# Kernel optimization log

Hardware: AMD Instinct MI355X
Metric: run time of the kernel (lower is better)

## Reference

```python
import jax, jax.numpy as jnp
import numpy as np

B, N, D = 4, 4096, 256
EPS = 1e-5


def setup_inputs() -> dict:
    key = jax.random.key(0)
    ks = jax.random.split(key, 6)
    x = jax.random.normal(ks[0], (B, N, D), dtype=jnp.float32)
    coord = jax.random.normal(ks[1], (B, N, D), dtype=jnp.float32)
    ln_g = jnp.ones((D,), dtype=jnp.float32)
    ln_b = jnp.zeros((D,), dtype=jnp.float32)
    s = 1.0 / np.sqrt(D)
    w_qkv = jax.random.normal(ks[2], (D, 3 * D), dtype=jnp.float32) * s
    w_out = jax.random.normal(ks[3], (D, D), dtype=jnp.float32) * s
    b_out = jnp.zeros((D,), dtype=jnp.float32)
    return {"x": x, "coord": coord, "ln_g": ln_g, "ln_b": ln_b,
            "w_qkv": w_qkv, "w_out": w_out, "b_out": b_out}


def reference(x, coord, ln_g, ln_b, w_qkv, w_out, b_out):
    d = x.shape[-1]
    scale = d ** (-0.5)
    # LayerNorm over last dim
    mu = jnp.mean(x, axis=-1, keepdims=True)
    var = jnp.var(x, axis=-1, keepdims=True)
    nx = (x - mu) * jax.lax.rsqrt(var + EPS) * ln_g + ln_b
    # QKV projection (no bias), chunk into q,k,v
    qkv = jnp.einsum('bnd,de->bne', nx, w_qkv)
    q, k, v = jnp.split(qkv, 3, axis=-1)
    # coord bias on q and k (module does NOT split into heads)
    q = q + coord
    k = k + coord
    dots = jnp.einsum('bnd,bmd->bnm', q, k) * scale
    attn = jax.nn.softmax(dots, axis=-1)
    out = jnp.einsum('bnm,bmd->bnd', attn, v)
    return jnp.einsum('bnd,de->bne', out, w_out) + b_out
```

## Files before the change

### kernel.cpp

```cpp
#include <hip/hip_runtime.h>
#include <hip/hip_fp16.h>
#include <math.h>

constexpr int B = 4, N = 4096, D = 256;
constexpr int BN = B * N;
constexpr float EPS = 1e-5f;
constexpr float QSC2 = 0.0625f * 1.44269504088896340736f;

constexpr int SPLIT = 4;
constexpr int KVB = 32;
constexpr int NTK = (N / SPLIT) / KVB;
constexpr float THR = 8.0f;

typedef __attribute__((ext_vector_type(8))) _Float16 f16x8;
typedef __attribute__((ext_vector_type(2))) __fp16 fp16x2;
typedef __attribute__((ext_vector_type(4))) float f32x4;
typedef __attribute__((ext_vector_type(16))) float f32x16;

__device__ inline f32x4 mfma_f16(f16x8 a, f16x8 b, f32x4 c) {
  return __builtin_amdgcn_mfma_f32_16x16x32_f16(a, b, c, 0, 0, 0);
}
__device__ inline f32x16 mfma32(f16x8 a, f16x8 b, f32x16 c) {
  return __builtin_amdgcn_mfma_f32_32x32x16_f16(a, b, c, 0, 0, 0);
}
__device__ inline ushort f2h(float x) {
  __half h = __float2half(x);
  return *(ushort*)&h;
}
__device__ inline float h2f(ushort u) {
  __half h;
  *(ushort*)&h = u;
  return __half2float(h);
}
__device__ inline unsigned pkh(float a, float b) {
  fp16x2 r = __builtin_amdgcn_cvt_pkrtz(a, b);
  return *(unsigned*)&r;
}
__device__ inline void gload16(const ushort* g, ushort* l) {
  __builtin_amdgcn_global_load_lds(
      (const __attribute__((address_space(1))) void*)g,
      (__attribute__((address_space(3))) void*)l, 16, 0, 0);
}

__global__ __launch_bounds__(256) void ln_kernel(
    const float* __restrict__ x, const float* __restrict__ g,
    const float* __restrict__ bta, ushort* __restrict__ nxh,
    ushort* __restrict__ nxl) {
  const int row = blockIdx.x;
  const int t = threadIdx.x;
  const float v = x[(size_t)row * D + t];
  float s = v, ss = v * v;
#pragma unroll
  for (int o = 32; o > 0; o >>= 1) {
    s += __shfl_down(s, o);
    ss += __shfl_down(ss, o);
  }
  __shared__ float red[8];
  if ((t & 63) == 0) {
    red[t >> 6] = s;
    red[(t >> 6) + 4] = ss;
  }
  __syncthreads();
  s = red[0] + red[1] + red[2] + red[3];
  ss = red[4] + red[5] + red[6] + red[7];
  const float mu = s * (1.0f / D);
  const float var = ss * (1.0f / D) - mu * mu;
  const float rsig = rsqrtf(var + EPS);
  const float nx = (v - mu) * rsig * g[t] + bta[t];
  const ushort h = f2h(nx);
  nxh[(size_t)row * D + t] = h;
  nxl[(size_t)row * D + t] = f2h(nx - h2f(h));
}

__global__ __launch_bounds__(256) void castw_kernel(
    const float* __restrict__ w_qkv, const float* __restrict__ w_out,
    ushort* __restrict__ wt, ushort* __restrict__ wot) {
  const int id = blockIdx.x * 256 + threadIdx.x;
  if (id < 768 * 256) {
    const int n = id >> 8, k = id & 255;
    wt[id] = f2h(w_qkv[(size_t)k * 768 + n]);
  } else {
    const int j = id - 768 * 256;
    const int n = j >> 8, k = j & 255;
    wot[j] = f2h(w_out[(size_t)k * 256 + n]);
  }
}

__global__ __launch_bounds__(256, 4) void qkv_kernel(
    const ushort* __restrict__ nxh, const ushort* __restrict__ nxl,
    const ushort* __restrict__ wt, const float* __restrict__ coord,
    ushort* __restrict__ qfp, ushort* __restrict__ kfp,
    ushort* __restrict__ vtp) {
  const int t = threadIdx.x;
  const int w = t >> 6, lane = t & 63;
  const int lrow = lane & 15, lhi = lane >> 4;
  const int m0 = blockIdx.x * 128 + w * 32;
  const int c0 = blockIdx.y * 64;
  f32x4 acc[2][4];
#pragma unroll
  for (int qs = 0; qs < 2; ++qs)
#pragma unroll
    for (int nt = 0; nt < 4; ++nt) acc[qs][nt] = f32x4{0.f, 0.f, 0.f, 0.f};

#pragma unroll
  for (int kc = 0; kc < D; kc += 32) {
    f16x8 ah[2], al[2], bw[4];
#pragma unroll
    for (int qs = 0; qs < 2; ++qs) {
      const size_t ao = (size_t)(m0 + qs * 16 + lrow) * D + kc + lhi * 8;
      ah[qs] = *(const f16x8*)(nxh + ao);
      al[qs] = *(const f16x8*)(nxl + ao);
    }
#pragma unroll
    for (int nt = 0; nt < 4; ++nt)
      bw[nt] = *(const f16x8*)(wt + (size_t)(c0 + nt * 16 + lrow) * D + kc +
                               lhi * 8);
#pragma unroll
    for (int qs = 0; qs < 2; ++qs)
#pragma unroll
      for (int nt = 0; nt < 4; ++nt) {
        acc[qs][nt] = mfma_f16(ah[qs], bw[nt], acc[qs][nt]);
        acc[qs][nt] = mfma_f16(al[qs], bw[nt], acc[qs][nt]);
      }
  }

  const int region = blockIdx.y >> 2;
  const int cbase = c0 & 255;
  if (region < 2) {
    const float sc = (region == 0) ? QSC2 : 1.0f;
    ushort* dp = (region == 0) ? qfp : kfp;
#pragma unroll
    for (int qs = 0; qs < 2; ++qs)
#pragma unroll
      for (int nt = 0; nt < 4; ++nt)
#pragma unroll
        for (int i = 0; i < 4; ++i) {
          const int row = m0 + qs * 16 + lhi * 4 + i;
          const int col = cbase + nt * 16 + lrow;
          const float val =
              (acc[qs][nt][i] + coord[(size_t)row * D + col]) * sc;
          dp[(size_t)row * D + col] = f2h(val);
        }
  } else {
#pragma unroll
    for (int qs = 0; qs < 2; ++qs)
#pragma unroll
      for (int nt = 0; nt < 4; ++nt)
#pragma unroll
        for (int i = 0; i < 4; ++i) {
          const int row = m0 + qs * 16 + lhi * 4 + i;
          const int col = cbase + nt * 16 + lrow;
          const int bb = row >> 12, n = row & (N - 1);
          vtp[((size_t)bb * D + col) * N + n] = f2h(acc[qs][nt][i]);
        }
  }
}

__global__ __launch_bounds__(512, 2) void attn_kernel(
    const ushort* __restrict__ qf, const ushort* __restrict__ kf,
    const ushort* __restrict__ vt, ushort* __restrict__ pob,
    float* __restrict__ mlb) {
  __shared__ ushort kbuf[3][8192];
  __shared__ ushort vbuf[3][8192];

  const int tid = threadIdx.x;
  const int lane = tid & 63;
  const int q = lane & 31, h = lane >> 5;
  const int w = tid >> 6;
  const int b = blockIdx.y, s = blockIdx.z;
  const int qw = blockIdx.x * 256 + w * 32;
  const int kbeg = s * (N / SPLIT);

  const ushort* qrow = qf + ((size_t)b * N + qw + q) * D;
  const ushort* kfb = kf + (size_t)b * N * D;
  const ushort* vtb = vt + (size_t)b * D * N;
  ushort* pog = pob + (size_t)s * BN * D;
  float* mlg = mlb + (size_t)s * BN * 2;

  f16x8 qfr[8];
#pragma unroll
  for (int c = 0; c < 8; ++c)
    qfr[c] = *(const f16x8*)(qrow + c * 16 + h * 8);

  f32x16 o[8];
#pragma unroll
  for (int dt = 0; dt < 8; ++dt)
#pragma unroll
    for (int r = 0; r < 16; ++r) o[dt][r] = 0.f;
  float m = -1e30f, lsum = 0.f;

  auto stage = [&](int bi, int k0) {
#pragma unroll
    for (int i = 0; i < 2; ++i) {
      const int g = i * 512 + tid;
      const int key = g >> 5, slot = g & 31;
      gload16(kfb + (size_t)(k0 + key) * D + ((slot ^ (key & 7)) * 8),
              &kbuf[bi][g * 8]);
    }
#pragma unroll
    for (int i = 0; i < 2; ++i) {
      const int g = i * 512 + tid;
      const int r = g >> 3, slot = g & 7;
      const int u = slot ^ (r & 7);
      const int d = r * 2 + (u >> 2);
      gload16(vtb + (size_t)d * N + k0 + ((u & 3) * 8), &vbuf[bi][g * 8]);
    }
  };

  stage(0, kbeg);

  for (int t = 0; t < NTK; ++t) {
    const int cur = t % 3;
    f16x8 qs[8];
#pragma unroll
    for (int c = 0; c < 8; ++c)
      qs[c] = *(const f16x8*)(qrow + (8 + c) * 16 + h * 8);
    if (t + 1 < NTK) {
      stage((t + 1) % 3, kbeg + (t + 1) * KVB);
      asm volatile("s_waitcnt vmcnt(12)" ::: "memory");
    } else {
      asm volatile("s_waitcnt vmcnt(8)" ::: "memory");
    }
    __builtin_amdgcn_sched_barrier(0);
    __builtin_amdgcn_s_barrier();
    __builtin_amdgcn_sched_barrier(0);

    f32x16 pa, pb;
#pragma unroll
    for (int r = 0; r < 16; ++r) { pa[r] = 0.f; pb[r] = 0.f; }
    const int ksw = (q & 7);
    __builtin_amdgcn_s_setprio(1);
#pragma unroll
    for (int c = 0; c < 8; ++c) {
      const f16x8 ka = *(const f16x8*)&kbuf[cur][q * 256 +
                                                 (((c * 2 + h) ^ ksw) * 8)];
      const f16x8 kb_ = *(const f16x8*)&kbuf[cur][q * 256 +
                                                  ((((c + 8) * 2 + h) ^ ksw) * 8)];
      pa = mfma32(ka, qfr[c], pa);
      pb = mfma32(kb_, qs[c], pb);
    }
    __builtin_amdgcn_s_setprio(0);
    f32x16 p;
#pragma unroll
    for (int r = 0; r < 16; ++r) p[r] = pa[r] + pb[r];

    float tm[8];
#pragma unroll
    for (int j = 0; j < 8; ++j) tm[j] = fmaxf(p[2 * j], p[2 * j + 1]);
    float pmax = fmaxf(fmaxf(fmaxf(tm[0], tm[1]), fmaxf(tm[2], tm[3])),
                       fmaxf(fmaxf(tm[4], tm[5]), fmaxf(tm[6], tm[7])));
    const float pm = fmaxf(pmax, __shfl_xor(pmax, 32));
    const bool need = pm > m + THR;
    if (__any(need)) {
      const float mn = fmaxf(m, pm);
      const float f = exp2f(m - mn);
      m = mn;
      lsum *= f;
#pragma unroll
      for (int dt = 0; dt < 8; ++dt) o[dt] *= f;
    }
#pragma unroll
    for (int r = 0; r < 16; ++r) {
      p[r] = exp2f(p[r] - m);
      lsum += p[r];
    }

    f16x8 pf[2];
#pragma unroll
    for (int kk = 0; kk < 2; ++kk) {
      const int sub = kk * 8;
      unsigned x = pkh(p[sub + 0], p[sub + 1]);
      unsigned z = pkh(p[sub + 2], p[sub + 3]);
      unsigned y = pkh(p[sub + 4], p[sub + 5]);
      unsigned wv = pkh(p[sub + 6], p[sub + 7]);
      const unsigned xs = __shfl_xor(x, 32);
      const unsigned zs = __shfl_xor(z, 32);
      const unsigned ys = __shfl_xor(y, 32);
      const unsigned ws = __shfl_xor(wv, 32);
      union { f16x8 v; unsigned u[4]; } pu;
      pu.u[0] = h ? ys : x;
      pu.u[1] = h ? ws : z;
      pu.u[2] = h ? y : xs;
      pu.u[3] = h ? wv : zs;
      pf[kk] = pu.v;
    }

    __builtin_amdgcn_s_setprio(1);
#pragma unroll
    for (int dt = 0; dt < 8; ++dt) {
      const int d = dt * 32 + q;
      const int rr = d >> 1;
#pragma unroll
      for (int kk = 0; kk < 2; ++kk) {
        const int u = (d & 1) * 4 + kk * 2 + h;
        const f16x8 vf = *(const f16x8*)&vbuf[cur][rr * 64 +
                                                   ((u ^ (rr & 7)) * 8)];
        o[dt] = mfma32(vf, pf[kk], o[dt]);
      }
    }
    __builtin_amdgcn_s_setprio(0);
  }

  const float lt = lsum + __shfl_xor(lsum, 32);
  const float inv = 1.0f / lt;
  ushort* orow = pog + ((size_t)b * N + qw + q) * D;
#pragma unroll
  for (int dt = 0; dt < 8; ++dt)
#pragma unroll
    for (int r4 = 0; r4 < 4; ++r4) {
      const unsigned u0 =
          pkh(o[dt][r4 * 4 + 0] * inv, o[dt][r4 * 4 + 1] * inv);
      const unsigned u1 =
          pkh(o[dt][r4 * 4 + 2] * inv, o[dt][r4 * 4 + 3] * inv);
      uint2 val;
      val.x = u0;
      val.y = u1;
      *(uint2*)(orow + dt * 32 + r4 * 8 + h * 4) = val;
    }
  if (h == 0) {
    const size_t r = (size_t)b * N + qw + q;
    mlg[r * 2] = m;
    mlg[r * 2 + 1] = lt;
  }
}

__global__ __launch_bounds__(256) void merge_kernel(
    const ushort* __restrict__ pob, const float* __restrict__ mlb,
    ushort* __restrict__ aoh, ushort* __restrict__ aol) {
  const int t = threadIdx.x;
  const int row = blockIdx.x * 8 + (t >> 5);
  const int d0 = (t & 31) * 8;
  float mv[SPLIT], lv[SPLIT];
  float mm = -1e30f;
#pragma unroll
  for (int s = 0; s < SPLIT; ++s) {
    mv[s] = mlb[(size_t)s * BN * 2 + row * 2];
    lv[s] = mlb[(size_t)s * BN * 2 + row * 2 + 1];
    mm = fmaxf(mm, mv[s]);
  }
  float wsum = 0.f, a[SPLIT];
#pragma unroll
  for (int s = 0; s < SPLIT; ++s) {
    a[s] = exp2f(mv[s] - mm) * lv[s];
    wsum += a[s];
  }
  const float invw = 1.0f / wsum;
  const size_t off = (size_t)row * D + d0;
  float r[8] = {};
#pragma unroll
  for (int s = 0; s < SPLIT; ++s) {
    const f16x8 p = *(const f16x8*)(pob + (size_t)s * BN * D + off);
    const float c = a[s] * invw;
#pragma unroll
    for (int j = 0; j < 8; ++j) r[j] += c * (float)p[j];
  }
  f16x8 rh, rl;
#pragma unroll
  for (int j = 0; j < 8; ++j) {
    rh[j] = (_Float16)r[j];
    rl[j] = (_Float16)(r[j] - (float)rh[j]);
  }
  *(f16x8*)(aoh + off) = rh;
  *(f16x8*)(aol + off) = rl;
}

__global__ __launch_bounds__(256, 4) void proj_kernel(
    const ushort* __restrict__ aoh, const ushort* __restrict__ aol,
    const ushort* __restrict__ wot, const float* __restrict__ bias,
    float* __restrict__ out) {
  const int t = threadIdx.x;
  const int w = t >> 6, lane = t & 63;
  const int lrow = lane & 15, lhi = lane >> 4;
  const int m0 = blockIdx.x * 128 + w * 32;
  const int c0 = blockIdx.y * 64;
  f32x4 acc[2][4];
#pragma unroll
  for (int qs = 0; qs < 2; ++qs)
#pragma unroll
    for (int nt = 0; nt < 4; ++nt) acc[qs][nt] = f32x4{0.f, 0.f, 0.f, 0.f};

#pragma unroll
  for (int kc = 0; kc < D; kc += 32) {
    f16x8 ah[2], al[2], bw[4];
#pragma unroll
    for (int qs = 0; qs < 2; ++qs) {
      const size_t ao = (size_t)(m0 + qs * 16 + lrow) * D + kc + lhi * 8;
      ah[qs] = *(const f16x8*)(aoh + ao);
      al[qs] = *(const f16x8*)(aol + ao);
    }
#pragma unroll
    for (int nt = 0; nt < 4; ++nt)
      bw[nt] = *(const f16x8*)(wot + (size_t)(c0 + nt * 16 + lrow) * D + kc +
                               lhi * 8);
#pragma unroll
    for (int qs = 0; qs < 2; ++qs)
#pragma unroll
      for (int nt = 0; nt < 4; ++nt) {
        acc[qs][nt] = mfma_f16(ah[qs], bw[nt], acc[qs][nt]);
        acc[qs][nt] = mfma_f16(al[qs], bw[nt], acc[qs][nt]);
      }
  }
#pragma unroll
  for (int qs = 0; qs < 2; ++qs)
#pragma unroll
    for (int nt = 0; nt < 4; ++nt)
#pragma unroll
      for (int i = 0; i < 4; ++i) {
        const int row = m0 + qs * 16 + lhi * 4 + i;
        const int col = c0 + nt * 16 + lrow;
        out[(size_t)row * D + col] = acc[qs][nt][i] + bias[col];
      }
}

extern "C" void kernel_launch(void* const* d_in, const int* in_sizes, int n_in,
                              void* d_out, int out_size, void* d_ws, size_t ws_size,
                              hipStream_t stream) {
  const float* x = (const float*)d_in[0];
  const float* coord = (const float*)d_in[1];
  const float* ln_g = (const float*)d_in[2];
  const float* ln_b = (const float*)d_in[3];
  const float* w_qkv = (const float*)d_in[4];
  const float* w_out = (const float*)d_in[5];
  const float* b_out = (const float*)d_in[6];
  float* out = (float*)d_out;

  const size_t P = (size_t)BN * D;

  ushort* qfp = (ushort*)d_ws;
  ushort* kfp = qfp + P;
  ushort* vtp = kfp + P;
  ushort* pob = vtp + P;
  float* mlb = (float*)(pob + (size_t)SPLIT * P);
  ushort* wt = (ushort*)(mlb + (size_t)SPLIT * BN * 2);
  ushort* wot = wt + 768 * 256;
  ushort* nxh = pob;
  ushort* nxl = pob + P;
  ushort* aoh = qfp;
  ushort* aol = kfp;

  hipLaunchKernelGGL(ln_kernel, dim3(BN), dim3(256), 0, stream,
                     x, ln_g, ln_b, nxh, nxl);
  hipLaunchKernelGGL(castw_kernel, dim3(1024), dim3(256), 0, stream,
                     w_qkv, w_out, wt, wot);
  hipLaunchKernelGGL(qkv_kernel, dim3(BN / 128, 12), dim3(256), 0, stream,
                     nxh, nxl, wt, coord, qfp, kfp, vtp);
  hipLaunchKernelGGL(attn_kernel, dim3(N / 256, B, SPLIT), dim3(512), 0,
                     stream, qfp, kfp, vtp, pob, mlb);
  hipLaunchKernelGGL(merge_kernel, dim3(BN / 8), dim3(256), 0, stream,
                     pob, mlb, aoh, aol);
  hipLaunchKernelGGL(proj_kernel, dim3(BN / 128, 4), dim3(256), 0, stream,
                     aoh, aol, wot, b_out, out);
}
```

Measured before the change: 203.8 us.

## Software-pipeline PV MFMA of previous tile behind current QK and softmax

```diff
diff --git a/kernel.cpp b/kernel.cpp
--- a/kernel.cpp
+++ b/kernel.cpp
@@ -160,8 +160,8 @@
     const ushort* __restrict__ qf, const ushort* __restrict__ kf,
     const ushort* __restrict__ vt, ushort* __restrict__ pob,
     float* __restrict__ mlb) {
-  __shared__ ushort kbuf[3][8192];
-  __shared__ ushort vbuf[3][8192];
+  __shared__ ushort kbuf[4][8192];
+  __shared__ ushort vbuf[4][8192];
 
   const int tid = threadIdx.x;
   const int lane = tid & 63;
@@ -188,6 +188,9 @@
 #pragma unroll
     for (int r = 0; r < 16; ++r) o[dt][r] = 0.f;
   float m = -1e30f, lsum = 0.f;
+  float f_prev = 1.0f;
+  bool need_prev = false;
+  f16x8 pf_prev[2];
 
   auto stage = [&](int bi, int k0) {
 #pragma unroll
@@ -210,13 +213,14 @@
   stage(0, kbeg);
 
   for (int t = 0; t < NTK; ++t) {
-    const int cur = t % 3;
+    const int cur = t & 3;
+    const int prv = (t + 3) & 3;
     f16x8 qs[8];
 #pragma unroll
     for (int c = 0; c < 8; ++c)
       qs[c] = *(const f16x8*)(qrow + (8 + c) * 16 + h * 8);
     if (t + 1 < NTK) {
-      stage((t + 1) % 3, kbeg + (t + 1) * KVB);
+      stage((t + 1) & 3, kbeg + (t + 1) * KVB);
       asm volatile("s_waitcnt vmcnt(12)" ::: "memory");
     } else {
       asm volatile("s_waitcnt vmcnt(8)" ::: "memory");
@@ -225,24 +229,40 @@
     __builtin_amdgcn_s_barrier();
     __builtin_amdgcn_sched_barrier(0);
 
-    f32x16 pa, pb;
-#pragma unroll
-    for (int r = 0; r < 16; ++r) { pa[r] = 0.f; pb[r] = 0.f; }
+    f32x16 p;
+#pragma unroll
+    for (int r = 0; r < 16; ++r) p[r] = 0.f;
     const int ksw = (q & 7);
     __builtin_amdgcn_s_setprio(1);
 #pragma unroll
-    for (int c = 0; c < 8; ++c) {
+    for (int c = 0; c < 16; ++c) {
+      const f16x8 qv = (c < 8) ? qfr[c] : qs[c - 8];
       const f16x8 ka = *(const f16x8*)&kbuf[cur][q * 256 +
                                                  (((c * 2 + h) ^ ksw) * 8)];
-      const f16x8 kb_ = *(const f16x8*)&kbuf[cur][q * 256 +
-                                                  ((((c + 8) * 2 + h) ^ ksw) * 8)];
-      pa = mfma32(ka, qfr[c], pa);
-      pb = mfma32(kb_, qs[c], pb);
+      p = mfma32(ka, qv, p);
     }
     __builtin_amdgcn_s_setprio(0);
-    f32x16 p;
-#pragma unroll
-    for (int r = 0; r < 16; ++r) p[r] = pa[r] + pb[r];
+
+    if (t > 0) {
+      if (need_prev) {
+#pragma unroll
+        for (int dt = 0; dt < 8; ++dt) o[dt] *= f_prev;
+      }
+      __builtin_amdgcn_s_setprio(1);
+#pragma unroll
+      for (int dt = 0; dt < 8; ++dt) {
+        const int d = dt * 32 + q;
+        const int rr = d >> 1;
+#pragma unroll
+        for (int kk = 0; kk < 2; ++kk) {
+          const int u = (d & 1) * 4 + kk * 2 + h;
+          const f16x8 vf = *(const f16x8*)&vbuf[prv][rr * 64 +
+                                                     ((u ^ (rr & 7)) * 8)];
+          o[dt] = mfma32(vf, pf_prev[kk], o[dt]);
+        }
+      }
+      __builtin_amdgcn_s_setprio(0);
+    }
 
     float tm[8];
 #pragma unroll
@@ -253,11 +273,12 @@
     const bool need = pm > m + THR;
     if (__any(need)) {
       const float mn = fmaxf(m, pm);
-      const float f = exp2f(m - mn);
+      f_prev = exp2f(m - mn);
       m = mn;
-      lsum *= f;
-#pragma unroll
-      for (int dt = 0; dt < 8; ++dt) o[dt] *= f;
+      lsum *= f_prev;
+      need_prev = true;
+    } else {
+      need_prev = false;
     }
 #pragma unroll
     for (int r = 0; r < 16; ++r) {
@@ -265,7 +286,6 @@
       lsum += p[r];
     }
 
-    f16x8 pf[2];
 #pragma unroll
     for (int kk = 0; kk < 2; ++kk) {
       const int sub = kk * 8;
@@ -282,10 +302,16 @@
       pu.u[1] = h ? ws : z;
       pu.u[2] = h ? y : xs;
       pu.u[3] = h ? wv : zs;
-      pf[kk] = pu.v;
-    }
-
-    __builtin_amdgcn_s_setprio(1);
+      pf_prev[kk] = pu.v;
+    }
+  }
+
+  if (need_prev) {
+#pragma unroll
+    for (int dt = 0; dt < 8; ++dt) o[dt] *= f_prev;
+  }
+  {
+    const int prv = (NTK - 1) & 3;
 #pragma unroll
     for (int dt = 0; dt < 8; ++dt) {
       const int d = dt * 32 + q;
@@ -293,14 +319,12 @@
 #pragma unroll
       for (int kk = 0; kk < 2; ++kk) {
         const int u = (d & 1) * 4 + kk * 2 + h;
-        const f16x8 vf = *(const f16x8*)&vbuf[cur][rr * 64 +
+        const f16x8 vf = *(const f16x8*)&vbuf[prv][rr * 64 +
                                                    ((u ^ (rr & 7)) * 8)];
-        o[dt] = mfma32(vf, pf[kk], o[dt]);
-      }
-    }
-    __builtin_amdgcn_s_setprio(0);
-  }
-
+        o[dt] = mfma32(vf, pf_prev[kk], o[dt]);
+      }
+    }
+  }
   const float lt = lsum + __shfl_xor(lsum, 32);
   const float inv = 1.0f / lt;
   ushort* orow = pog + ((size_t)b * N + qw + q) * D;
```

New measurement: 195.2 us. -4.2%, faster.
